# Performance work log

Measured on AMD Instinct MI355X. Metric: run time of the kernel, lower is better.

## Reference

```python
import jax, jax.numpy as jnp
import numpy as np

FEATURE_DIM, HIDDEN_DIM, ATTN_DIM = 2048, 1024, 1024
B, L = 128, 196


def setup_inputs() -> dict:
    key = jax.random.key(0)
    ks = jax.random.split(key, 8)
    s_enc = 1.0 / np.sqrt(FEATURE_DIM)
    s_hid = 1.0 / np.sqrt(HIDDEN_DIM)
    s_full = 1.0 / np.sqrt(ATTN_DIM)
    return {
        "encoder_out": jax.random.normal(ks[0], (B, L, FEATURE_DIM), jnp.float32),
        "hidden": jax.random.normal(ks[1], (B, HIDDEN_DIM), jnp.float32),
        "W_enc": jax.random.uniform(ks[2], (FEATURE_DIM, ATTN_DIM), jnp.float32, -s_enc, s_enc),
        "b_enc": jax.random.uniform(ks[3], (ATTN_DIM,), jnp.float32, -s_enc, s_enc),
        "W_hid": jax.random.uniform(ks[4], (HIDDEN_DIM, ATTN_DIM), jnp.float32, -s_hid, s_hid),
        "b_hid": jax.random.uniform(ks[5], (ATTN_DIM,), jnp.float32, -s_hid, s_hid),
        "W_full": jax.random.uniform(ks[6], (ATTN_DIM,), jnp.float32, -s_full, s_full),
        "b_full": jax.random.uniform(ks[7], (1,), jnp.float32, -s_full, s_full),
    }


def reference(encoder_out, hidden, W_enc, b_enc, W_hid, b_hid, W_full, b_full):
    # attn1: (B, L, A)
    attn1 = jnp.einsum("blf,fa->bla", encoder_out, W_enc) + b_enc
    # attn2: (B, 1, A)
    attn2 = (hidden @ W_hid + b_hid)[:, None, :]
    attn = jax.nn.relu(attn1 + attn2)
    # scalar score per location: (B, L)
    scores = jnp.einsum("bla,a->bl", attn, W_full) + b_full[0]
    alpha = jax.nn.softmax(scores, axis=1)
    # weighted sum over L: (B, F)
    context = jnp.einsum("blf,bl->bf", encoder_out, alpha)
    return context, alpha
```

## Files before the change

### kernel.cpp

```cpp
#include <hip/hip_runtime.h>
#include <hip/hip_bf16.h>

typedef unsigned short u16;
typedef short s16x8 __attribute__((ext_vector_type(8)));
typedef unsigned int u32x2 __attribute__((ext_vector_type(2)));
typedef unsigned int u32x4 __attribute__((ext_vector_type(4)));
typedef float f32x4 __attribute__((ext_vector_type(4)));

#define F_DIM 2048
#define A_DIM 1024
#define H_DIM 1024
#define BATCH 128
#define LLEN  196
#define MROWS (BATCH * LLEN)
#define MTILES (MROWS / 256)

__device__ __forceinline__ u16 f2b(float x) {
  union { float f; unsigned int u; } c; c.f = x;
  unsigned int r = (c.u + 0x7fffu + ((c.u >> 16) & 1u)) >> 16;
  return (u16)r;
}

__device__ __forceinline__ unsigned int f2b_pk(float a, float b) {
  unsigned int r;
  asm volatile("v_cvt_pk_bf16_f32 %0, %1, %2" : "=v"(r) : "v"(a), "v"(b));
  return r;
}

__device__ __forceinline__ void gload_lds16(const void* g, void* l) {
  __builtin_amdgcn_global_load_lds((const __attribute__((address_space(1))) void*)g,
                                   (__attribute__((address_space(3))) void*)l, 16, 0, 0);
}

__global__ __launch_bounds__(256) void prep_kernel(
    const float* __restrict__ W, u16* __restrict__ WT,
    const float* __restrict__ hidden, const float* __restrict__ W_hid,
    const float* __restrict__ b_hid, const float* __restrict__ b_enc,
    float* __restrict__ attn2p,
    const float* __restrict__ enc, u16* __restrict__ encB) {
  int t = threadIdx.x;
  if (blockIdx.x < 2048) {
    __shared__ float tile[32][33];
    int id = blockIdx.x;
    int kb = (id & 63) * 32, ab = (id >> 6) * 32;
    int r = t >> 3, c = (t & 7) * 4;
    float4 v = *(const float4*)&W[(size_t)(kb + r) * A_DIM + ab + c];
    tile[r][c] = v.x; tile[r][c + 1] = v.y; tile[r][c + 2] = v.z; tile[r][c + 3] = v.w;
    __syncthreads();
    ushort4 o;
    o.x = f2b(tile[c + 0][r]);
    o.y = f2b(tile[c + 1][r]);
    o.z = f2b(tile[c + 2][r]);
    o.w = f2b(tile[c + 3][r]);
    *(ushort4*)&WT[(size_t)(ab + r) * F_DIM + kb + c] = o;
  } else if (blockIdx.x < 2560) {
    __shared__ float hl[8][128];
    int id = blockIdx.x - 2048;
    int a  = (id & 3) * 256 + t;
    int b0 = ((id >> 2) & 15) * 8;
    int k0 = (id >> 6) * 128;
    {
      int j = t >> 5, kk = (t & 31) * 4;
      float4 v = *(const float4*)&hidden[(size_t)(b0 + j) * H_DIM + k0 + kk];
      hl[j][kk + 0] = v.x; hl[j][kk + 1] = v.y; hl[j][kk + 2] = v.z; hl[j][kk + 3] = v.w;
    }
    __syncthreads();
    float acc[8] = {0.f, 0.f, 0.f, 0.f, 0.f, 0.f, 0.f, 0.f};
    #pragma unroll 4
    for (int k = 0; k < 128; ++k) {
      float w = W_hid[(size_t)(k0 + k) * A_DIM + a];
      #pragma unroll
      for (int j = 0; j < 8; ++j) acc[j] = fmaf(hl[j][k], w, acc[j]);
    }
    if ((id >> 6) == 0) {
      float bias = b_hid[a] + b_enc[a];
      #pragma unroll
      for (int j = 0; j < 8; ++j) acc[j] += bias;
    }
    #pragma unroll
    for (int j = 0; j < 8; ++j) atomicAdd(&attn2p[(size_t)(b0 + j) * A_DIM + a], acc[j]);
  } else {
    int r = blockIdx.x - 2560;
    const float4* sp = (const float4*)(enc + (size_t)r * F_DIM) + t * 2;
    float4 a = sp[0], b = sp[1];
    u32x4 w;
    w.x = f2b_pk(a.x, a.y); w.y = f2b_pk(a.z, a.w);
    w.z = f2b_pk(b.x, b.y); w.w = f2b_pk(b.z, b.w);
    *(u32x4*)(encB + (size_t)r * F_DIM + t * 8) = w;
  }
}

__global__ __launch_bounds__(512, 2) void gemm_score_a(
    const u16* __restrict__ encB, const u16* __restrict__ WT,
    const float* __restrict__ attn2p, const float* __restrict__ W_full,
    float* __restrict__ scores) {
  __shared__ __align__(16) u16 As[2 * 16384];
  __shared__ __align__(16) u16 Bs[2 * 16384];

  int i = blockIdx.x;
  int g = i >> 5, r = i & 31;
  int y = r >> 3, gi = r & 7;
  int mt = g * 8 + gi;
  if (mt >= MTILES) return;
  int m0 = mt * 256, n0 = y * 256;
  int t = threadIdx.x;
  int lane = t & 63, wave = t >> 6;
  int wr = wave >> 2, wc = wave & 3;
  int c16 = lane & 15, quad = lane >> 4;

  const u16* agp = encB + (size_t)(m0 + (t >> 3)) * F_DIM + ((t & 7) ^ ((t >> 3) & 7)) * 8;
  const u16* bgp = WT   + (size_t)(n0 + (t >> 3)) * F_DIM + ((t & 7) ^ ((t >> 3) & 7)) * 8;

  const int akey = c16 & 7;
  int gsw[2];
  gsw[0] = ((0 * 4 + quad) ^ akey) * 8;
  gsw[1] = ((1 * 4 + quad) ^ akey) * 8;
  const int aro = (wr * 128 + c16) * 64;
  const int bro = (wc * 64 + c16) * 64;

  f32x4 acc[8][4];
  #pragma unroll
  for (int mi = 0; mi < 8; ++mi)
    #pragma unroll
    for (int ni = 0; ni < 4; ++ni) acc[mi][ni] = (f32x4){0.f, 0.f, 0.f, 0.f};

  s16x8 af[4][2], bf0[2][2], bf1[2][2];

#define AGL(cb, kt_) do {                                                       \
    _Pragma("unroll")                                                           \
    for (int s_ = 0; s_ < 4; ++s_)                                              \
      gload_lds16(agp + (size_t)s_ * 64 * F_DIM + (size_t)(kt_) * 64,           \
                  As + (cb) * 16384 + s_ * 4096 + wave * 512);                  \
  } while (0)

#define BGL(cb, kt_) do {                                                       \
    _Pragma("unroll")                                                           \
    for (int s_ = 0; s_ < 4; ++s_)                                              \
      gload_lds16(bgp + (size_t)s_ * 64 * F_DIM + (size_t)(kt_) * 64,           \
                  Bs + (cb) * 16384 + s_ * 4096 + wave * 512);                  \
  } while (0)

#define DSRA(cb, mh)                                                            \
    _Pragma("unroll")                                                           \
    for (int i_ = 0; i_ < 4; ++i_)                                              \
      _Pragma("unroll")                                                         \
      for (int h_ = 0; h_ < 2; ++h_)                                            \
        af[i_][h_] = *(const s16x8*)&As[(cb) * 16384 + aro                      \
                                        + ((mh) * 4 + i_) * 1024 + gsw[h_]];

#define DSRB(BF, cb, nh)                                                        \
    _Pragma("unroll")                                                           \
    for (int j_ = 0; j_ < 2; ++j_)                                              \
      _Pragma("unroll")                                                         \
      for (int h_ = 0; h_ < 2; ++h_)                                            \
        BF[j_][h_] = *(const s16x8*)&Bs[(cb) * 16384 + bro                      \
                                        + ((nh) * 2 + j_) * 1024 + gsw[h_]];

#define PHTAIL(BF, mh, nh) do {                                                 \
    __builtin_amdgcn_s_barrier();                                               \
    asm volatile("s_waitcnt lgkmcnt(0)" ::: "memory");                          \
    __builtin_amdgcn_s_setprio(1);                                              \
    _Pragma("unroll")                                                           \
    for (int i_ = 0; i_ < 4; ++i_)                                              \
      _Pragma("unroll")                                                         \
      for (int j_ = 0; j_ < 2; ++j_)                                            \
        _Pragma("unroll")                                                       \
        for (int h_ = 0; h_ < 2; ++h_)                                          \
          acc[(mh) * 4 + i_][(nh) * 2 + j_] =                                   \
              __builtin_amdgcn_mfma_f32_16x16x32_bf16(                          \
                  af[i_][h_], BF[j_][h_],                                       \
                  acc[(mh) * 4 + i_][(nh) * 2 + j_], 0, 0, 0);                  \
    __builtin_amdgcn_s_setprio(0);                                              \
    __builtin_amdgcn_s_barrier();                                               \
  } while (0)

#define GROUPA(T_, RB_, WB_) do {                                               \
    int kS_ = min((T_) + 1, 31);                                                \
     DSRA(RB_, 0); DSRB(bf0, RB_, 0); AGL(WB_, kS_); PHTAIL(bf0, 0, 0);\
     DSRB(bf1, RB_, 1); BGL(WB_, kS_);              PHTAIL(bf1, 0, 1); \
     DSRA(RB_, 1);                                   PHTAIL(bf0, 1, 0);\
     asm volatile("s_waitcnt vmcnt(0)" ::: "memory"); PHTAIL(bf1, 1, 1);\
  } while (0)

  AGL(0, 0);
  BGL(0, 0);
  asm volatile("s_waitcnt vmcnt(0) lgkmcnt(0)" ::: "memory");
  __builtin_amdgcn_s_barrier();

  #pragma unroll 1
  for (int T = 0; T < 32; T += 2) {
    GROUPA(T,     0, 1);
    GROUPA(T + 1, 1, 0);
  }
#undef GROUPA
#undef PHTAIL
#undef DSRA
#undef DSRB
#undef BGL
#undef AGL

  int bfirst = m0 / LLEN;
  int bnd1 = (bfirst + 1) * LLEN, bnd2 = (bfirst + 2) * LLEN;
  int b1c = min(bfirst + 1, BATCH - 1), b2c = min(bfirst + 2, BATCH - 1);
  float wf[4], a2v0[4], a2v1[4], a2v2[4];
  #pragma unroll
  for (int ni = 0; ni < 4; ++ni) {
    int col = n0 + wc * 64 + ni * 16 + c16;
    wf[ni]   = W_full[col];
    a2v0[ni] = attn2p[(size_t)bfirst * A_DIM + col];
    a2v1[ni] = attn2p[(size_t)b1c * A_DIM + col];
    a2v2[ni] = attn2p[(size_t)b2c * A_DIM + col];
  }
  #pragma unroll
  for (int mi = 0; mi < 8; ++mi) {
    #pragma unroll
    for (int rr = 0; rr < 4; ++rr) {
      int row_g = m0 + wr * 128 + mi * 16 + quad * 4 + rr;
      float p = 0.f;
      #pragma unroll
      for (int ni = 0; ni < 4; ++ni) {
        float a2 = row_g >= bnd1 ? (row_g >= bnd2 ? a2v2[ni] : a2v1[ni]) : a2v0[ni];
        float v = acc[mi][ni][rr] + a2;
        v = fmaxf(v, 0.f);
        p = fmaf(v, wf[ni], p);
      }
      p += __shfl_xor(p, 1);
      p += __shfl_xor(p, 2);
      p += __shfl_xor(p, 4);
      p += __shfl_xor(p, 8);
      if (c16 == 0) atomicAdd(&scores[row_g], p);
    }
  }
}

__global__ __launch_bounds__(512, 2) void gemm_score_b(
    const float* __restrict__ enc, const u16* __restrict__ WT,
    const float* __restrict__ attn2p, const float* __restrict__ W_full,
    float* __restrict__ scores) {
  __shared__ __align__(16) u16 As[2 * 16384];
  __shared__ __align__(16) u16 Bs[2 * 16384];

  int i = blockIdx.x;
  int g = i >> 5, r = i & 31;
  int y = r >> 3, gi = r & 7;
  int mt = g * 8 + gi;
  if (mt >= MTILES) return;
  int m0 = mt * 256, n0 = y * 256;
  int t = threadIdx.x;
  int lane = t & 63, wave = t >> 6;
  int wr = wave >> 2, wc = wave & 3;
  int c16 = lane & 15, quad = lane >> 4;

  const float* aP = enc + (size_t)(m0 + (t >> 2)) * F_DIM + (t & 3) * 4;
  int awo[4];
  #pragma unroll
  for (int s = 0; s < 4; ++s)
    awo[s] = (t >> 2) * 64 + ((t & 3) & 1) * 4
           + (((s * 2 + ((t & 3) >> 1)) ^ ((t >> 2) & 7)) * 8);
  const u16* bgp = WT + (size_t)(n0 + (t >> 3)) * F_DIM + ((t & 7) ^ ((t >> 3) & 7)) * 8;

  const int akey = c16 & 7;
  int gsw[2];
  gsw[0] = ((0 * 4 + quad) ^ akey) * 8;
  gsw[1] = ((1 * 4 + quad) ^ akey) * 8;
  const int aro = (wr * 128 + c16) * 64;
  const int bro = (wc * 64 + c16) * 64;

  f32x4 acc[8][4];
  #pragma unroll
  for (int mi = 0; mi < 8; ++mi)
    #pragma unroll
    for (int ni = 0; ni < 4; ++ni) acc[mi][ni] = (f32x4){0.f, 0.f, 0.f, 0.f};

  s16x8 af[4][2], bf[2][2];
  float4 R0lo[4], R0hi[4], R1lo[4], R1hi[4];

#define ALD(RX, half, kt_) do {                                                 \
    const float* p_ = aP + (size_t)(half) * 128 * F_DIM + (kt_) * 64;           \
    RX[0] = *(const float4*)(p_);                                               \
    RX[1] = *(const float4*)(p_ + 16);                                          \
    RX[2] = *(const float4*)(p_ + 32);                                          \
    RX[3] = *(const float4*)(p_ + 48);                                          \
  } while (0)

#define AWR(RX, cb, half) do {                                                  \
    _Pragma("unroll")                                                           \
    for (int s_ = 0; s_ < 4; ++s_) {                                            \
      u32x2 w_; w_.x = f2b_pk(RX[s_].x, RX[s_].y);                              \
      w_.y = f2b_pk(RX[s_].z, RX[s_].w);                                        \
      *(u32x2*)&As[(cb) * 16384 + (half) * 8192 + awo[s_]] = w_;                \
    }                                                                           \
  } while (0)

#define BGL(cb, kt_) do {                                                       \
    _Pragma("unroll")                                                           \
    for (int s_ = 0; s_ < 4; ++s_)                                              \
      gload_lds16(bgp + (size_t)s_ * 64 * F_DIM + (size_t)(kt_) * 64,           \
                  Bs + (cb) * 16384 + s_ * 4096 + wave * 512);                  \
  } while (0)

#define DSRA(cb, mh)                                                            \
    _Pragma("unroll")                                                           \
    for (int i_ = 0; i_ < 4; ++i_)                                              \
      _Pragma("unroll")                                                         \
      for (int h_ = 0; h_ < 2; ++h_)                                            \
        af[i_][h_] = *(const s16x8*)&As[(cb) * 16384 + aro                      \
                                        + ((mh) * 4 + i_) * 1024 + gsw[h_]];

#define DSRB(cb, nh)                                                            \
    _Pragma("unroll")                                                           \
    for (int j_ = 0; j_ < 2; ++j_)                                              \
      _Pragma("unroll")                                                         \
      for (int h_ = 0; h_ < 2; ++h_)                                            \
        bf[j_][h_] = *(const s16x8*)&Bs[(cb) * 16384 + bro                      \
                                        + ((nh) * 2 + j_) * 1024 + gsw[h_]];

#define PHTAIL(mh, nh) do {                                                     \
    __builtin_amdgcn_s_barrier();                                               \
    asm volatile("s_waitcnt lgkmcnt(0)" ::: "memory");                          \
    __builtin_amdgcn_s_setprio(1);                                              \
    _Pragma("unroll")                                                           \
    for (int i_ = 0; i_ < 4; ++i_)                                              \
      _Pragma("unroll")                                                         \
      for (int j_ = 0; j_ < 2; ++j_)                                            \
        _Pragma("unroll")                                                       \
        for (int h_ = 0; h_ < 2; ++h_)                                          \
          acc[(mh) * 4 + i_][(nh) * 2 + j_] =                                   \
              __builtin_amdgcn_mfma_f32_16x16x32_bf16(                          \
                  af[i_][h_], bf[j_][h_],                                       \
                  acc[(mh) * 4 + i_][(nh) * 2 + j_], 0, 0, 0);                  \
    __builtin_amdgcn_s_setprio(0);                                               \
    __builtin_amdgcn_s_barrier();                                               \
  } while (0)

#define GROUP(T_, RB_, WB_, WLO_, WHI_, LLO_, LHI_) do {                        \
    int kB_ = min((T_) + 1, 31);                                                \
    int kA_ = min((T_) + 2, 31);                                                \
     DSRA(RB_, 0); DSRB(RB_, 0); AWR(WLO_, WB_, 0); BGL(WB_, kB_);      \
    PHTAIL(0, 0);                                                               \
     DSRB(RB_, 1); AWR(WHI_, WB_, 1); ALD(LLO_, 0, kA_);                \
    PHTAIL(0, 1);                                                               \
     DSRA(RB_, 1); DSRB(RB_, 0); ALD(LHI_, 1, kA_);                     \
    PHTAIL(1, 0);                                                               \
     DSRB(RB_, 1);                                                      \
    asm volatile("s_waitcnt vmcnt(8)" ::: "memory");                            \
    PHTAIL(1, 1);                                                               \
  } while (0)

  ALD(R0lo, 0, 0);
  ALD(R0hi, 1, 0);
  BGL(0, 0);
  asm volatile("s_waitcnt vmcnt(4)" ::: "memory");
  AWR(R0lo, 0, 0);
  AWR(R0hi, 0, 1);
  ALD(R1lo, 0, 1);
  ALD(R1hi, 1, 1);
  asm volatile("s_waitcnt vmcnt(8) lgkmcnt(0)" ::: "memory");
  __builtin_amdgcn_s_barrier();

  #pragma unroll 1
  for (int T = 0; T < 32; T += 2) {
    GROUP(T,     0, 1, R1lo, R1hi, R0lo, R0hi);
    GROUP(T + 1, 1, 0, R0lo, R0hi, R1lo, R1hi);
  }
#undef GROUP
#undef PHTAIL
#undef DSRA
#undef DSRB
#undef BGL
#undef AWR
#undef ALD

  int bfirst = m0 / LLEN;
  int bnd1 = (bfirst + 1) * LLEN, bnd2 = (bfirst + 2) * LLEN;
  int b1c = min(bfirst + 1, BATCH - 1), b2c = min(bfirst + 2, BATCH - 1);
  float wf[4], a2v0[4], a2v1[4], a2v2[4];
  #pragma unroll
  for (int ni = 0; ni < 4; ++ni) {
    int col = n0 + wc * 64 + ni * 16 + c16;
    wf[ni]   = W_full[col];
    a2v0[ni] = attn2p[(size_t)bfirst * A_DIM + col];
    a2v1[ni] = attn2p[(size_t)b1c * A_DIM + col];
    a2v2[ni] = attn2p[(size_t)b2c * A_DIM + col];
  }
  #pragma unroll
  for (int mi = 0; mi < 8; ++mi) {
    #pragma unroll
    for (int rr = 0; rr < 4; ++rr) {
      int row_g = m0 + wr * 128 + mi * 16 + quad * 4 + rr;
      float p = 0.f;
      #pragma unroll
      for (int ni = 0; ni < 4; ++ni) {
        float a2 = row_g >= bnd1 ? (row_g >= bnd2 ? a2v2[ni] : a2v1[ni]) : a2v0[ni];
        float v = acc[mi][ni][rr] + a2;
        v = fmaxf(v, 0.f);
        p = fmaf(v, wf[ni], p);
      }
      p += __shfl_xor(p, 1);
      p += __shfl_xor(p, 2);
      p += __shfl_xor(p, 4);
      p += __shfl_xor(p, 8);
      if (c16 == 0) atomicAdd(&scores[row_g], p);
    }
  }
}

__global__ __launch_bounds__(256) void context_kernel(
    const float* __restrict__ enc, const float* __restrict__ scores,
    float* __restrict__ alpha_out, float* __restrict__ out) {
  __shared__ float al[LLEN];
  __shared__ float red[8];
  __shared__ float4 part[4][64];
  int b = blockIdx.y, t = threadIdx.x;
  float s = (t < LLEN) ? scores[b * LLEN + t] : -3.0e38f;
  float m = s;
  #pragma unroll
  for (int o = 1; o <= 32; o <<= 1) m = fmaxf(m, __shfl_xor(m, o));
  if ((t & 63) == 0) red[t >> 6] = m;
  __syncthreads();
  m = fmaxf(fmaxf(red[0], red[1]), fmaxf(red[2], red[3]));
  float e = (t < LLEN) ? expf(s - m) : 0.f;
  float sum = e;
  #pragma unroll
  for (int o = 1; o <= 32; o <<= 1) sum += __shfl_xor(sum, o);
  if ((t & 63) == 0) red[4 + (t >> 6)] = sum;
  __syncthreads();
  sum = red[4] + red[5] + red[6] + red[7];
  float av = e / sum;
  if (t < LLEN) {
    al[t] = av;
    if (blockIdx.x == 0) alpha_out[b * LLEN + t] = av;
  }
  __syncthreads();
  int f4 = blockIdx.x * 64 + (t & 63);
  int lq = t >> 6;
  const float4* e4 = (const float4*)enc
                   + ((size_t)b * LLEN + lq * 49) * (F_DIM / 4) + f4;
  float4 acc = {0.f, 0.f, 0.f, 0.f};
  #pragma unroll 7
  for (int j = 0; j < 49; ++j) {
    float4 v = e4[(size_t)j * (F_DIM / 4)];
    float a = al[lq * 49 + j];
    acc.x = fmaf(v.x, a, acc.x);
    acc.y = fmaf(v.y, a, acc.y);
    acc.z = fmaf(v.z, a, acc.z);
    acc.w = fmaf(v.w, a, acc.w);
  }
  part[lq][t & 63] = acc;
  __syncthreads();
  if (t < 64) {
    float4 p0 = part[0][t], p1 = part[1][t], p2 = part[2][t], p3 = part[3][t];
    float4 sv;
    sv.x = (p0.x + p1.x) + (p2.x + p3.x);
    sv.y = (p0.y + p1.y) + (p2.y + p3.y);
    sv.z = (p0.z + p1.z) + (p2.z + p3.z);
    sv.w = (p0.w + p1.w) + (p2.w + p3.w);
    *(float4*)(out + (size_t)b * F_DIM + (size_t)(blockIdx.x * 64 + t) * 4) = sv;
  }
}

extern "C" void kernel_launch(void* const* d_in, const int* in_sizes, int n_in,
                              void* d_out, int out_size, void* d_ws, size_t ws_size,
                              hipStream_t stream) {
  const float* enc    = (const float*)d_in[0];
  const float* hidden = (const float*)d_in[1];
  const float* W_enc  = (const float*)d_in[2];
  const float* b_enc  = (const float*)d_in[3];
  const float* W_hid  = (const float*)d_in[4];
  const float* b_hid  = (const float*)d_in[5];
  const float* W_full = (const float*)d_in[6];
  float* out = (float*)d_out;
  float* alpha_out = out + (size_t)BATCH * F_DIM;

  const size_t wt_bytes   = (size_t)A_DIM * F_DIM * sizeof(u16);
  const size_t a2_bytes   = (size_t)BATCH * A_DIM * sizeof(float);
  const size_t sc_bytes   = (size_t)MROWS * sizeof(float);
  const size_t encb_bytes = (size_t)MROWS * F_DIM * sizeof(u16);
  char* ws = (char*)d_ws;
  u16*   WT     = (u16*)ws;
  float* attn2p = (float*)(ws + wt_bytes);
  float* scores = (float*)(ws + wt_bytes + a2_bytes);
  u16*   encB   = (u16*)(ws + wt_bytes + a2_bytes + sc_bytes);

  const bool bigws = ws_size >= wt_bytes + a2_bytes + sc_bytes + encb_bytes;

  hipMemsetAsync(attn2p, 0, a2_bytes + sc_bytes, stream);

  if (bigws) {
    prep_kernel<<<dim3(2048 + 512 + MROWS), 256, 0, stream>>>(
        W_enc, WT, hidden, W_hid, b_hid, b_enc, attn2p, enc, encB);
    gemm_score_a<<<dim3(416), 512, 0, stream>>>(encB, WT, attn2p, W_full, scores);
  } else {
    prep_kernel<<<dim3(2048 + 512), 256, 0, stream>>>(
        W_enc, WT, hidden, W_hid, b_hid, b_enc, attn2p, enc, encB);
    gemm_score_b<<<dim3(416), 512, 0, stream>>>(enc, WT, attn2p, W_full, scores);
  }
  context_kernel<<<dim3(8, BATCH), 256, 0, stream>>>(enc, scores, alpha_out, out);
}
```

Before: 470.9 us.

## Deepen GEMM pipeline to 4 stages with K=32 tiles; grid-stride bf16 conversion

```diff
diff --git a/kernel.cpp b/kernel.cpp
--- a/kernel.cpp
+++ b/kernel.cpp
@@ -80,13 +80,16 @@
     #pragma unroll
     for (int j = 0; j < 8; ++j) atomicAdd(&attn2p[(size_t)(b0 + j) * A_DIM + a], acc[j]);
   } else {
-    int r = blockIdx.x - 2560;
-    const float4* sp = (const float4*)(enc + (size_t)r * F_DIM) + t * 2;
-    float4 a = sp[0], b = sp[1];
-    u32x4 w;
-    w.x = f2b_pk(a.x, a.y); w.y = f2b_pk(a.z, a.w);
-    w.z = f2b_pk(b.x, b.y); w.w = f2b_pk(b.z, b.w);
-    *(u32x4*)(encB + (size_t)r * F_DIM + t * 8) = w;
+    const size_t n8 = (size_t)MROWS * F_DIM / 8;
+    size_t gid = (size_t)(blockIdx.x - 2560) * 256 + t;
+    for (size_t k = gid; k < n8; k += (size_t)2048 * 256) {
+      const float4* sp = (const float4*)enc + k * 2;
+      float4 a = sp[0], b = sp[1];
+      u32x4 w;
+      w.x = f2b_pk(a.x, a.y); w.y = f2b_pk(a.z, a.w);
+      w.z = f2b_pk(b.x, b.y); w.w = f2b_pk(b.z, b.w);
+      *(u32x4*)(encB + k * 8) = w;
+    }
   }
 }
 
@@ -94,8 +97,8 @@
     const u16* __restrict__ encB, const u16* __restrict__ WT,
     const float* __restrict__ attn2p, const float* __restrict__ W_full,
     float* __restrict__ scores) {
-  __shared__ __align__(16) u16 As[2 * 16384];
-  __shared__ __align__(16) u16 Bs[2 * 16384];
+  __shared__ __align__(16) u16 As[4 * 8192];
+  __shared__ __align__(16) u16 Bs[4 * 8192];
 
   int i = blockIdx.x;
   int g = i >> 5, r = i & 31;
@@ -108,15 +111,12 @@
   int wr = wave >> 2, wc = wave & 3;
   int c16 = lane & 15, quad = lane >> 4;
 
-  const u16* agp = encB + (size_t)(m0 + (t >> 3)) * F_DIM + ((t & 7) ^ ((t >> 3) & 7)) * 8;
-  const u16* bgp = WT   + (size_t)(n0 + (t >> 3)) * F_DIM + ((t & 7) ^ ((t >> 3) & 7)) * 8;
-
-  const int akey = c16 & 7;
-  int gsw[2];
-  gsw[0] = ((0 * 4 + quad) ^ akey) * 8;
-  gsw[1] = ((1 * 4 + quad) ^ akey) * 8;
-  const int aro = (wr * 128 + c16) * 64;
-  const int bro = (wc * 64 + c16) * 64;
+  const u16* agp = encB + (size_t)(m0 + (t >> 2)) * F_DIM + ((t & 3) ^ ((t >> 3) & 3)) * 8;
+  const u16* bgp = WT   + (size_t)(n0 + (t >> 2)) * F_DIM + ((t & 3) ^ ((t >> 3) & 3)) * 8;
+
+  const int gsw = (quad ^ ((c16 >> 1) & 3)) * 8;
+  const int aro = (wr * 128 + c16) * 32;
+  const int bro = (wc * 64 + c16) * 32;
 
   f32x4 acc[8][4];
   #pragma unroll
@@ -124,75 +124,68 @@
     #pragma unroll
     for (int ni = 0; ni < 4; ++ni) acc[mi][ni] = (f32x4){0.f, 0.f, 0.f, 0.f};
 
-  s16x8 af[4][2], bf0[2][2], bf1[2][2];
+  s16x8 af[4], bf[4];
 
 #define AGL(cb, kt_) do {                                                       \
     _Pragma("unroll")                                                           \
-    for (int s_ = 0; s_ < 4; ++s_)                                              \
-      gload_lds16(agp + (size_t)s_ * 64 * F_DIM + (size_t)(kt_) * 64,           \
-                  As + (cb) * 16384 + s_ * 4096 + wave * 512);                  \
+    for (int s_ = 0; s_ < 2; ++s_)                                              \
+      gload_lds16(agp + (size_t)s_ * 128 * F_DIM + (size_t)(kt_) * 32,          \
+                  As + (cb) * 8192 + s_ * 4096 + wave * 512);                   \
   } while (0)
 
 #define BGL(cb, kt_) do {                                                       \
     _Pragma("unroll")                                                           \
-    for (int s_ = 0; s_ < 4; ++s_)                                              \
-      gload_lds16(bgp + (size_t)s_ * 64 * F_DIM + (size_t)(kt_) * 64,           \
-                  Bs + (cb) * 16384 + s_ * 4096 + wave * 512);                  \
+    for (int s_ = 0; s_ < 2; ++s_)                                              \
+      gload_lds16(bgp + (size_t)s_ * 128 * F_DIM + (size_t)(kt_) * 32,          \
+                  Bs + (cb) * 8192 + s_ * 4096 + wave * 512);                   \
   } while (0)
 
 #define DSRA(cb, mh)                                                            \
     _Pragma("unroll")                                                           \
     for (int i_ = 0; i_ < 4; ++i_)                                              \
-      _Pragma("unroll")                                                         \
-      for (int h_ = 0; h_ < 2; ++h_)                                            \
-        af[i_][h_] = *(const s16x8*)&As[(cb) * 16384 + aro                      \
-                                        + ((mh) * 4 + i_) * 1024 + gsw[h_]];
-
-#define DSRB(BF, cb, nh)                                                        \
-    _Pragma("unroll")                                                           \
-    for (int j_ = 0; j_ < 2; ++j_)                                              \
-      _Pragma("unroll")                                                         \
-      for (int h_ = 0; h_ < 2; ++h_)                                            \
-        BF[j_][h_] = *(const s16x8*)&Bs[(cb) * 16384 + bro                      \
-                                        + ((nh) * 2 + j_) * 1024 + gsw[h_]];
-
-#define PHTAIL(BF, mh, nh) do {                                                 \
+      af[i_] = *(const s16x8*)&As[(cb) * 8192 + aro + ((mh) * 4 + i_) * 512 + gsw];
+
+#define DSRB(cb)                                                                \
+    _Pragma("unroll")                                                           \
+    for (int j_ = 0; j_ < 4; ++j_)                                              \
+      bf[j_] = *(const s16x8*)&Bs[(cb) * 8192 + bro + j_ * 512 + gsw];
+
+#define PHTAIL(mh) do {                                                         \
     __builtin_amdgcn_s_barrier();                                               \
     asm volatile("s_waitcnt lgkmcnt(0)" ::: "memory");                          \
     __builtin_amdgcn_s_setprio(1);                                              \
     _Pragma("unroll")                                                           \
     for (int i_ = 0; i_ < 4; ++i_)                                              \
       _Pragma("unroll")                                                         \
-      for (int j_ = 0; j_ < 2; ++j_)                                            \
-        _Pragma("unroll")                                                       \
-        for (int h_ = 0; h_ < 2; ++h_)                                          \
-          acc[(mh) * 4 + i_][(nh) * 2 + j_] =                                   \
-              __builtin_amdgcn_mfma_f32_16x16x32_bf16(                          \
-                  af[i_][h_], BF[j_][h_],                                       \
-                  acc[(mh) * 4 + i_][(nh) * 2 + j_], 0, 0, 0);                  \
+      for (int j_ = 0; j_ < 4; ++j_)                                            \
+        acc[(mh) * 4 + i_][j_] =                                                \
+            __builtin_amdgcn_mfma_f32_16x16x32_bf16(                            \
+                af[i_], bf[j_], acc[(mh) * 4 + i_][j_], 0, 0, 0);               \
     __builtin_amdgcn_s_setprio(0);                                              \
     __builtin_amdgcn_s_barrier();                                               \
   } while (0)
 
-#define GROUPA(T_, RB_, WB_) do {                                               \
-    int kS_ = min((T_) + 1, 31);                                                \
-     DSRA(RB_, 0); DSRB(bf0, RB_, 0); AGL(WB_, kS_); PHTAIL(bf0, 0, 0);\
-     DSRB(bf1, RB_, 1); BGL(WB_, kS_);              PHTAIL(bf1, 0, 1); \
-     DSRA(RB_, 1);                                   PHTAIL(bf0, 1, 0);\
-     asm volatile("s_waitcnt vmcnt(0)" ::: "memory"); PHTAIL(bf1, 1, 1);\
-  } while (0)
-
-  AGL(0, 0);
-  BGL(0, 0);
-  asm volatile("s_waitcnt vmcnt(0) lgkmcnt(0)" ::: "memory");
+#define TILE(T_, RB_, WB_) do {                                                 \
+    int kS_ = min((T_) + 2, 63);                                                \
+     DSRA(RB_, 0); DSRB(RB_); AGL(WB_, kS_); PHTAIL(0);                 \
+     DSRA(RB_, 1); BGL(WB_, kS_);                                       \
+    asm volatile("s_waitcnt vmcnt(4)" ::: "memory");                            \
+    PHTAIL(1);                                                                  \
+  } while (0)
+
+  AGL(0, 0); BGL(0, 0);
+  AGL(1, 1); BGL(1, 1);
+  asm volatile("s_waitcnt vmcnt(4)" ::: "memory");
   __builtin_amdgcn_s_barrier();
 
   #pragma unroll 1
-  for (int T = 0; T < 32; T += 2) {
-    GROUPA(T,     0, 1);
-    GROUPA(T + 1, 1, 0);
-  }
-#undef GROUPA
+  for (int T = 0; T < 64; T += 4) {
+    TILE(T,     0, 2);
+    TILE(T + 1, 1, 3);
+    TILE(T + 2, 2, 0);
+    TILE(T + 3, 3, 1);
+  }
+#undef TILE
 #undef PHTAIL
 #undef DSRA
 #undef DSRB
@@ -329,7 +322,7 @@
               __builtin_amdgcn_mfma_f32_16x16x32_bf16(                          \
                   af[i_][h_], bf[j_][h_],                                       \
                   acc[(mh) * 4 + i_][(nh) * 2 + j_], 0, 0, 0);                  \
-    __builtin_amdgcn_s_setprio(0);                                               \
+    __builtin_amdgcn_s_setprio(0);                                              \
     __builtin_amdgcn_s_barrier();                                               \
   } while (0)
 
@@ -487,7 +480,7 @@
   hipMemsetAsync(attn2p, 0, a2_bytes + sc_bytes, stream);
 
   if (bigws) {
-    prep_kernel<<<dim3(2048 + 512 + MROWS), 256, 0, stream>>>(
+    prep_kernel<<<dim3(2048 + 512 + 2048), 256, 0, stream>>>(
         W_enc, WT, hidden, W_hid, b_hid, b_enc, attn2p, enc, encB);
     gemm_score_a<<<dim3(416), 512, 0, stream>>>(encB, WT, attn2p, W_full, scores);
   } else {
```

Result: no change. 476.6 us (+1.2%).
